# Kernel optimization log

Measured on AMD Instinct MI355X. Metric: run time of the kernel, lower is better.

## Reference

```python
import jax, jax.numpy as jnp
import numpy as np

TEMPERATURE = 0.5
BN_EPS = 1e-5
L2_EPS = 1e-12

B, D_IN, D_HID, D_OUT = 4096, 192, 512, 128


def setup_inputs() -> dict:
    key = jax.random.key(0)
    ks = jax.random.split(key, 4)
    return {
        "h1": jax.random.normal(ks[0], (B, D_IN), dtype=jnp.float32),
        "h2": jax.random.normal(ks[1], (B, D_IN), dtype=jnp.float32),
        "W1": jax.random.normal(ks[2], (D_HID, D_IN), dtype=jnp.float32) * (1.0 / np.sqrt(D_IN)),
        "b1": jnp.zeros((D_HID,), dtype=jnp.float32),
        "gamma": jnp.ones((D_HID,), dtype=jnp.float32),
        "beta": jnp.zeros((D_HID,), dtype=jnp.float32),
        "W2": jax.random.normal(ks[3], (D_OUT, D_HID), dtype=jnp.float32) * (1.0 / np.sqrt(D_HID)),
        "b2": jnp.zeros((D_OUT,), dtype=jnp.float32),
    }


def _projection_head(h, W1, b1, gamma, beta, W2, b2):
    # Linear -> BatchNorm1d (training-mode batch stats) -> ReLU -> Linear
    y = h @ W1.T + b1  # (B, D_HID)
    mean = jnp.mean(y, axis=0)
    var = jnp.mean((y - mean) ** 2, axis=0)  # biased var, as torch BN uses for normalization
    y = (y - mean) * jax.lax.rsqrt(var + BN_EPS) * gamma + beta
    y = jax.nn.relu(y)
    return y @ W2.T + b2  # (B, D_OUT)


def _l2_normalize(z):
    n = jnp.sqrt(jnp.sum(z * z, axis=1, keepdims=True))
    return z / jnp.maximum(n, L2_EPS)


def reference(h1, h2, W1, b1, gamma, beta, W2, b2):
    z1 = _l2_normalize(_projection_head(h1, W1, b1, gamma, beta, W2, b2))
    z2 = _l2_normalize(_projection_head(h2, W1, b1, gamma, beta, W2, b2))

    # NT-Xent, fully vectorized (equivalent to the per-row torch loop):
    z = jnp.concatenate([z1, z2], axis=0)            # (2B, D)
    sim = (z @ z.T) / TEMPERATURE                    # (2B, 2B)
    n2 = z.shape[0]
    sim = jnp.where(jnp.eye(n2, dtype=bool), -jnp.inf, sim)
    # positive pair similarity: sim[i, i+B] and sim[i+B, i] == z1_i . z2_i / T
    pos = jnp.sum(z1 * z2, axis=1) / TEMPERATURE     # (B,)
    pos = jnp.concatenate([pos, pos])                # (2B,)
    # excluding index i from the row equals including it since diag is -inf
    lse = jax.nn.logsumexp(sim, axis=1)              # (2B,)
    loss = jnp.mean(lse - pos)
    return loss, z1, z2
```

## Files before the change

### kernel.cpp

```cpp
#include <hip/hip_runtime.h>


#define NB   4096
#define DIN  192
#define DHID 512
#define DOUT 128
#define N2   8192
#define NSPLIT 32
#define SIM_ITERS 16

typedef short short8 __attribute__((ext_vector_type(8)));
typedef float floatx4 __attribute__((ext_vector_type(4)));

__device__ inline float fast_exp2(float x) {
#if __has_builtin(__builtin_amdgcn_exp2f)
    return __builtin_amdgcn_exp2f(x);
#else
    return exp2f(x);
#endif
}

__device__ inline unsigned short bf16_rne(float x) {
    unsigned int u = __float_as_uint(x);
    return (unsigned short)((u + 0x7fffu + ((u >> 16) & 1u)) >> 16);
}

__global__ __launch_bounds__(256) void prep(
    const float* __restrict__ W1, const float* __restrict__ W2,
    unsigned short* __restrict__ W1b, unsigned short* __restrict__ W2b,
    float* __restrict__ psumc, float* __restrict__ psqc, float* __restrict__ out)
{
    const int NW1 = DHID * DIN / 4;
    const int NW2 = DOUT * DHID / 4;
    if (blockIdx.x == 160) {
        int t = threadIdx.x;
        for (int i = t; i < 1024; i += 256) { psumc[i] = 0.f; psqc[i] = 0.f; }
        if (t == 0) out[0] = 0.f;
        return;
    }
    int id = blockIdx.x * 256 + threadIdx.x;
    const float* src; unsigned short* dst; int off;
    if (id < NW1)            { src = W1; dst = W1b; off = id; }
    else if (id < NW1 + NW2) { src = W2; dst = W2b; off = id - NW1; }
    else return;
    float4 x = ((const float4*)src)[off];
    unsigned int p0 = bf16_rne(x.x) | ((unsigned int)bf16_rne(x.y) << 16);
    unsigned int p1 = bf16_rne(x.z) | ((unsigned int)bf16_rne(x.w) << 16);
    ((uint2*)dst)[off] = make_uint2(p0, p1);
}

__global__ __launch_bounds__(256) void gemm1_mfma(
    const float* __restrict__ h1, const float* __restrict__ h2,
    const unsigned short* __restrict__ W1b, const float* __restrict__ b1,
    float* __restrict__ Y, float* __restrict__ psumc, float* __restrict__ psqc)
{
    const int t = threadIdx.x;
    const int wave = t >> 6, lane = t & 63;
    const int quad = lane >> 4, l15 = lane & 15;
    const int mb = blockIdx.x;
    const int m0 = mb * 128 + wave * 32;
    const int n0 = blockIdx.y * 64;
    const int v  = (mb >= 32);

    short8 a[2][6];
    #pragma unroll
    for (int mt = 0; mt < 2; ++mt) {
        int row = m0 + mt * 16 + l15;
        const float* hsrc = (row < NB) ? (h1 + (size_t)row * DIN)
                                       : (h2 + (size_t)(row - NB) * DIN);
        #pragma unroll
        for (int kc = 0; kc < 6; ++kc) {
            const float4* p = (const float4*)(hsrc + kc * 32 + quad * 8);
            float4 x0 = p[0], x1 = p[1];
            float xs[8] = {x0.x,x0.y,x0.z,x0.w,x1.x,x1.y,x1.z,x1.w};
            #pragma unroll
            for (int j = 0; j < 8; ++j) a[mt][kc][j] = (short)bf16_rne(xs[j]);
        }
    }

    #pragma unroll
    for (int nt = 0; nt < 4; ++nt) {
        const int col = n0 + nt * 16 + l15;
        const short8* bptr = (const short8*)(W1b + (size_t)col * DIN + quad * 8);
        short8 b[6];
        #pragma unroll
        for (int kc = 0; kc < 6; ++kc) b[kc] = bptr[kc * 4];
        floatx4 acc[2] = {{0.f,0.f,0.f,0.f},{0.f,0.f,0.f,0.f}};
        #pragma unroll
        for (int kc = 0; kc < 6; ++kc)
            #pragma unroll
            for (int mt = 0; mt < 2; ++mt)
                acc[mt] = __builtin_amdgcn_mfma_f32_16x16x32_bf16(a[mt][kc], b[kc], acc[mt], 0,0,0);
        const float bias = b1[col];
        float cs = 0.f, cq = 0.f;
        #pragma unroll
        for (int mt = 0; mt < 2; ++mt)
            #pragma unroll
            for (int reg = 0; reg < 4; ++reg) {
                float y = acc[mt][reg] + bias;
                int row = m0 + mt * 16 + quad * 4 + reg;
                Y[(size_t)row * DHID + col] = y;
                cs += y; cq += y * y;
            }
        cs += __shfl_xor(cs, 16); cs += __shfl_xor(cs, 32);
        cq += __shfl_xor(cq, 16); cq += __shfl_xor(cq, 32);
        if (quad == 0) {
            atomicAdd(psumc + v * DHID + col, cs);
            atomicAdd(psqc  + v * DHID + col, cq);
        }
    }
}

#define ZSCALE 1.6986436f

__global__ __launch_bounds__(256) void gemm2_mfma(
    const float* __restrict__ Y, const unsigned short* __restrict__ W2b,
    const float* __restrict__ psumc, const float* __restrict__ psqc,
    const float* __restrict__ gamma, const float* __restrict__ beta,
    const float* __restrict__ b2,
    unsigned short* __restrict__ Zb, float* __restrict__ outz)
{
    __shared__ float sc_sh[DHID], sh_sh[DHID];
    __shared__ float sq_lds[4][16];
    const int t = threadIdx.x;
    const int wave = t >> 6, lane = t & 63;
    const int quad = lane >> 4, l15 = lane & 15;
    const int mtbase = blockIdx.x * 16;
    const int v = (mtbase >= NB);

    for (int c = t; c < DHID; c += 256) {
        float mean = psumc[v * DHID + c] * (1.0f / NB);
        float var  = psqc [v * DHID + c] * (1.0f / NB) - mean * mean;
        float rstd = rsqrtf(var + 1e-5f);
        float scv = gamma[c] * rstd;
        sc_sh[c] = scv;
        sh_sh[c] = beta[c] - mean * scv;
    }
    __syncthreads();

    const float* yrow = Y + (size_t)(mtbase + l15) * DHID;
    floatx4 acc[2] = {{0.f,0.f,0.f,0.f},{0.f,0.f,0.f,0.f}};
    for (int kc = 0; kc < 16; ++kc) {
        const int k = kc * 32 + quad * 8;
        float4 y0 = *(const float4*)(yrow + k);
        float4 y1 = *(const float4*)(yrow + k + 4);
        float4 s0 = *(const float4*)&sc_sh[k], s1 = *(const float4*)&sc_sh[k + 4];
        float4 h0 = *(const float4*)&sh_sh[k], h1v = *(const float4*)&sh_sh[k + 4];
        float xs[8];
        xs[0] = fmaxf(y0.x * s0.x + h0.x, 0.f);
        xs[1] = fmaxf(y0.y * s0.y + h0.y, 0.f);
        xs[2] = fmaxf(y0.z * s0.z + h0.z, 0.f);
        xs[3] = fmaxf(y0.w * s0.w + h0.w, 0.f);
        xs[4] = fmaxf(y1.x * s1.x + h1v.x, 0.f);
        xs[5] = fmaxf(y1.y * s1.y + h1v.y, 0.f);
        xs[6] = fmaxf(y1.z * s1.z + h1v.z, 0.f);
        xs[7] = fmaxf(y1.w * s1.w + h1v.w, 0.f);
        short8 a;
        #pragma unroll
        for (int j = 0; j < 8; ++j) a[j] = (short)bf16_rne(xs[j]);
        #pragma unroll
        for (int nt = 0; nt < 2; ++nt) {
            const int col = wave * 32 + nt * 16 + l15;
            short8 b = *(const short8*)(W2b + (size_t)col * DHID + k);
            acc[nt] = __builtin_amdgcn_mfma_f32_16x16x32_bf16(a, b, acc[nt], 0,0,0);
        }
    }
    float bias[2];
    #pragma unroll
    for (int nt = 0; nt < 2; ++nt) bias[nt] = b2[wave * 32 + nt * 16 + l15];

    float zv[4][2];
    #pragma unroll
    for (int reg = 0; reg < 4; ++reg) {
        float sq = 0.f;
        #pragma unroll
        for (int nt = 0; nt < 2; ++nt) {
            zv[reg][nt] = acc[nt][reg] + bias[nt];
            sq += zv[reg][nt] * zv[reg][nt];
        }
        sq += __shfl_xor(sq, 1); sq += __shfl_xor(sq, 2);
        sq += __shfl_xor(sq, 4); sq += __shfl_xor(sq, 8);
        if (l15 == 0) sq_lds[wave][quad * 4 + reg] = sq;
    }
    __syncthreads();
    #pragma unroll
    for (int reg = 0; reg < 4; ++reg) {
        float tot = sq_lds[0][quad * 4 + reg] + sq_lds[1][quad * 4 + reg]
                  + sq_lds[2][quad * 4 + reg] + sq_lds[3][quad * 4 + reg];
        float inv = 1.0f / fmaxf(sqrtf(tot), 1e-12f);
        const int row = mtbase + quad * 4 + reg;
        const size_t ob = (size_t)row * DOUT;
        #pragma unroll
        for (int nt = 0; nt < 2; ++nt) {
            const int col = wave * 32 + nt * 16 + l15;
            float z = zv[reg][nt] * inv;
            outz[ob + col] = z;
            Zb[ob + col] = bf16_rne(z * ZSCALE);
        }
    }
}

__global__ __launch_bounds__(256, 2) void sim_mfma(
    const unsigned short* __restrict__ Zb, float* __restrict__ psum)
{
    __shared__ unsigned char bsh[65536];
    const int t = threadIdx.x;
    const int wave = t >> 6, lane = t & 63;
    const int quad = lane >> 4, l15 = lane & 15;
    const int mbase = blockIdx.x * 128 + wave * 32;
    const int cs = blockIdx.y;
    const int cbase = cs * (N2 / NSPLIT);

    {
        const uint4* src = (const uint4*)(Zb + (size_t)cbase * DOUT);
        #pragma unroll
        for (int k = 0; k < 16; ++k) {
            int idx = t + k * 256;
            uint4 vv = src[idx];
            int row  = idx >> 4;
            int slot = idx & 15;
            *(uint4*)(bsh + row * 256 + ((slot ^ (row & 15)) << 4)) = vv;
        }
    }

    short8 a[2][4];
    #pragma unroll
    for (int at = 0; at < 2; ++at) {
        const short8* zra = (const short8*)(Zb + (size_t)(mbase + at * 16 + l15) * DOUT + quad * 8);
        #pragma unroll
        for (int kc = 0; kc < 4; ++kc) a[at][kc] = zra[kc * 4];
    }

    float rs[2][4];
    #pragma unroll
    for (int at = 0; at < 2; ++at)
        #pragma unroll
        for (int r = 0; r < 4; ++r) rs[at][r] = 0.f;

    __syncthreads();

    #pragma unroll 1
    for (int nt = 0; nt < SIM_ITERS; ++nt) {
        const int crow = nt * 16 + l15;
        short8 b[4];
        #pragma unroll
        for (int kc = 0; kc < 4; ++kc) {
            int slot = kc * 4 + quad;
            int boff = crow * 256 + ((slot ^ (crow & 15)) << 4);
            b[kc] = *(const short8*)(bsh + boff);
        }

        floatx4 acc[2] = {{0.f,0.f,0.f,0.f},{0.f,0.f,0.f,0.f}};
        #pragma unroll
        for (int kc = 0; kc < 4; ++kc)
            #pragma unroll
            for (int at = 0; at < 2; ++at)
                acc[at] = __builtin_amdgcn_mfma_f32_16x16x32_bf16(a[at][kc], b[kc], acc[at], 0, 0, 0);

        #pragma unroll
        for (int at = 0; at < 2; ++at)
            #pragma unroll
            for (int r = 0; r < 4; ++r)
                rs[at][r] += fast_exp2(acc[at][r]);
    }

    #pragma unroll
    for (int at = 0; at < 2; ++at) {
        const int gi0 = mbase + at * 16 + quad * 4;
        #pragma unroll
        for (int r = 0; r < 4; ++r) {
            float s = rs[at][r];
            s += __shfl_xor(s, 1);
            s += __shfl_xor(s, 2);
            s += __shfl_xor(s, 4);
            s += __shfl_xor(s, 8);
            if (l15 == 0) psum[(size_t)cs * N2 + gi0 + r] = s;
        }
    }
}

__global__ __launch_bounds__(256) void row_finalize(
    const unsigned short* __restrict__ Zb, const float* __restrict__ psum,
    float* __restrict__ out)
{
    const int t = threadIdx.x, wave = t >> 6, lane = t & 63;
    const int half = lane >> 5, l5 = lane & 31;
    const unsigned int* Z32 = (const unsigned int*)Zb;
    const int gw = blockIdx.x * 4 + wave;
    float accrv = 0.f;

    #pragma unroll 1
    for (int pp = 0; pp < 4; ++pp) {
        const int k = gw * 4 + pp;
        float s = psum[(size_t)l5 * N2 + k + half * NB];
        s += __shfl_xor(s, 1); s += __shfl_xor(s, 2); s += __shfl_xor(s, 4);
        s += __shfl_xor(s, 8); s += __shfl_xor(s, 16);
        unsigned int aw = Z32[(size_t)k * 64 + lane];
        unsigned int bw = Z32[(size_t)(k + NB) * 64 + lane];
        float alo = __uint_as_float(aw << 16), ahi = __uint_as_float(aw & 0xffff0000u);
        float blo = __uint_as_float(bw << 16), bhi = __uint_as_float(bw & 0xffff0000u);
        float d12 = alo * blo + ahi * bhi;
        float d11 = alo * alo + ahi * ahi;
        float d22 = blo * blo + bhi * bhi;
        #pragma unroll
        for (int m = 1; m <= 32; m <<= 1) {
            d12 += __shfl_xor(d12, m);
            d11 += __shfl_xor(d11, m);
            d22 += __shfl_xor(d22, m);
        }
        if (l5 == 0) {
            float dself = half ? d22 : d11;
            accrv += logf(s - fast_exp2(dself)) - d12 * 0.69314718f;
        }
    }
    accrv += __shfl_xor(accrv, 32);
    __shared__ float wsr[4];
    if (lane == 0) wsr[wave] = accrv;
    __syncthreads();
    if (t == 0)
        atomicAdd(out, (wsr[0] + wsr[1] + wsr[2] + wsr[3]) * (1.0f / N2));
}

extern "C" void kernel_launch(void* const* d_in, const int* in_sizes, int n_in,
                              void* d_out, int out_size, void* d_ws, size_t ws_size,
                              hipStream_t stream)
{
    const float* h1    = (const float*)d_in[0];
    const float* h2    = (const float*)d_in[1];
    const float* W1    = (const float*)d_in[2];
    const float* b1    = (const float*)d_in[3];
    const float* gamma = (const float*)d_in[4];
    const float* beta  = (const float*)d_in[5];
    const float* W2    = (const float*)d_in[6];
    const float* b2    = (const float*)d_in[7];
    float* out = (float*)d_out;

    float* ws      = (float*)d_ws;
    float* psumc   = ws;
    float* psqc    = psumc + 1024;
    unsigned short* W1b = (unsigned short*)(psqc + 1024);
    unsigned short* W2b = W1b + DHID * DIN;
    float* Y       = (float*)(W2b + DOUT * DHID);
    float* psum    = Y + (size_t)N2 * DHID;
    unsigned short* Zb = (unsigned short*)(psum + (size_t)NSPLIT * N2);

    prep        <<<dim3(161),        256, 0, stream>>>(W1, W2, W1b, W2b, psumc, psqc, out);
    gemm1_mfma  <<<dim3(64, 8),      256, 0, stream>>>(h1, h2, W1b, b1, Y, psumc, psqc);
    gemm2_mfma  <<<dim3(512),        256, 0, stream>>>(Y, W2b, psumc, psqc, gamma, beta, b2, Zb, out + 1);
    sim_mfma    <<<dim3(64, NSPLIT), 256, 0, stream>>>(Zb, psum);
    row_finalize<<<dim3(256),        256, 0, stream>>>(Zb, psum, out);
}
```

Baseline: 141.4 us.

## Exploit symmetry of similarity matrix to compute only upper-triangular tiles

The similarity kernel now iterates over upper-triangular 256x256 super-tile pairs instead of the full 8192x8192 grid. Each off-diagonal tile adds its exp values both to its row sums and, through an LDS column reduction, to the column sums of the mirrored rows. Results are accumulated with atomics into a single per-row sum buffer, which removes the split partial-sum array and its reduction in the finalize kernel. This roughly halves the MFMA and exp work, at the cost of extra shuffles, LDS updates, atomics and float summation order that is no longer deterministic.

```diff
diff --git a/kernel.cpp b/kernel.cpp
--- a/kernel.cpp
+++ b/kernel.cpp
@@ -6,7 +6,7 @@
 #define DHID 512
 #define DOUT 128
 #define N2   8192
-#define NSPLIT 32
+#define NSUPER 32
 #define SIM_ITERS 16
 
 typedef short short8 __attribute__((ext_vector_type(8)));
@@ -28,13 +28,15 @@
 __global__ __launch_bounds__(256) void prep(
     const float* __restrict__ W1, const float* __restrict__ W2,
     unsigned short* __restrict__ W1b, unsigned short* __restrict__ W2b,
-    float* __restrict__ psumc, float* __restrict__ psqc, float* __restrict__ out)
+    float* __restrict__ psumc, float* __restrict__ psqc,
+    float* __restrict__ out, float* __restrict__ psum_row)
 {
     const int NW1 = DHID * DIN / 4;
     const int NW2 = DOUT * DHID / 4;
     if (blockIdx.x == 160) {
         int t = threadIdx.x;
         for (int i = t; i < 1024; i += 256) { psumc[i] = 0.f; psqc[i] = 0.f; }
+        for (int i = t; i < N2; i += 256)   psum_row[i] = 0.f;
         if (t == 0) out[0] = 0.f;
         return;
     }
@@ -201,15 +203,29 @@
 }
 
 __global__ __launch_bounds__(256, 2) void sim_mfma(
-    const unsigned short* __restrict__ Zb, float* __restrict__ psum)
+    const unsigned short* __restrict__ Zb, float* __restrict__ psum_row)
 {
     __shared__ unsigned char bsh[65536];
+    __shared__ float colsum[4][256];
     const int t = threadIdx.x;
     const int wave = t >> 6, lane = t & 63;
     const int quad = lane >> 4, l15 = lane & 15;
-    const int mbase = blockIdx.x * 128 + wave * 32;
-    const int cs = blockIdx.y;
-    const int cbase = cs * (N2 / NSPLIT);
+
+    int R, C, half;
+    {
+        int id = blockIdx.x;
+        if (id < 2 * NSUPER) { R = id >> 1; C = R; half = id & 1; }
+        else {
+            int p2 = id - 2 * NSUPER;
+            int pair = p2 >> 1; half = p2 & 1;
+            int r = 0, rem = pair;
+            while (rem >= NSUPER - 1 - r) { rem -= NSUPER - 1 - r; ++r; }
+            R = r; C = r + 1 + rem;
+        }
+    }
+    const bool docol = (C != R);
+    const int mbase = R * 256 + half * 128 + wave * 32;
+    const int cbase = C * 256;
 
     {
         const uint4* src = (const uint4*)(Zb + (size_t)cbase * DOUT);
@@ -221,6 +237,8 @@
             int slot = idx & 15;
             *(uint4*)(bsh + row * 256 + ((slot ^ (row & 15)) << 4)) = vv;
         }
+        #pragma unroll
+        for (int w = 0; w < 4; ++w) colsum[w][t] = 0.f;
     }
 
     short8 a[2][4];
@@ -257,12 +275,23 @@
             for (int at = 0; at < 2; ++at)
                 acc[at] = __builtin_amdgcn_mfma_f32_16x16x32_bf16(a[at][kc], b[kc], acc[at], 0, 0, 0);
 
+        float cst = 0.f;
         #pragma unroll
         for (int at = 0; at < 2; ++at)
             #pragma unroll
-            for (int r = 0; r < 4; ++r)
-                rs[at][r] += fast_exp2(acc[at][r]);
-    }
+            for (int r = 0; r < 4; ++r) {
+                float e = fast_exp2(acc[at][r]);
+                rs[at][r] += e;
+                cst += e;
+            }
+        if (docol) {
+            cst += __shfl_xor(cst, 16);
+            cst += __shfl_xor(cst, 32);
+            if (quad == 0) colsum[wave][nt * 16 + l15] += cst;
+        }
+    }
+
+    __syncthreads();
 
     #pragma unroll
     for (int at = 0; at < 2; ++at) {
@@ -274,13 +303,17 @@
             s += __shfl_xor(s, 2);
             s += __shfl_xor(s, 4);
             s += __shfl_xor(s, 8);
-            if (l15 == 0) psum[(size_t)cs * N2 + gi0 + r] = s;
-        }
+            if (l15 == 0) atomicAdd(psum_row + gi0 + r, s);
+        }
+    }
+    if (docol) {
+        float tot = colsum[0][t] + colsum[1][t] + colsum[2][t] + colsum[3][t];
+        atomicAdd(psum_row + cbase + t, tot);
     }
 }
 
 __global__ __launch_bounds__(256) void row_finalize(
-    const unsigned short* __restrict__ Zb, const float* __restrict__ psum,
+    const unsigned short* __restrict__ Zb, const float* __restrict__ psum_row,
     float* __restrict__ out)
 {
     const int t = threadIdx.x, wave = t >> 6, lane = t & 63;
@@ -292,9 +325,6 @@
     #pragma unroll 1
     for (int pp = 0; pp < 4; ++pp) {
         const int k = gw * 4 + pp;
-        float s = psum[(size_t)l5 * N2 + k + half * NB];
-        s += __shfl_xor(s, 1); s += __shfl_xor(s, 2); s += __shfl_xor(s, 4);
-        s += __shfl_xor(s, 8); s += __shfl_xor(s, 16);
         unsigned int aw = Z32[(size_t)k * 64 + lane];
         unsigned int bw = Z32[(size_t)(k + NB) * 64 + lane];
         float alo = __uint_as_float(aw << 16), ahi = __uint_as_float(aw & 0xffff0000u);
@@ -309,6 +339,7 @@
             d22 += __shfl_xor(d22, m);
         }
         if (l5 == 0) {
+            float s = psum_row[k + half * NB];
             float dself = half ? d22 : d11;
             accrv += logf(s - fast_exp2(dself)) - d12 * 0.69314718f;
         }
@@ -341,12 +372,14 @@
     unsigned short* W1b = (unsigned short*)(psqc + 1024);
     unsigned short* W2b = W1b + DHID * DIN;
     float* Y       = (float*)(W2b + DOUT * DHID);
-    float* psum    = Y + (size_t)N2 * DHID;
-    unsigned short* Zb = (unsigned short*)(psum + (size_t)NSPLIT * N2);
-
-    prep        <<<dim3(161),        256, 0, stream>>>(W1, W2, W1b, W2b, psumc, psqc, out);
+    float* psum_row= Y + (size_t)N2 * DHID;
+    unsigned short* Zb = (unsigned short*)(psum_row + N2);
+
+    const int SIM_BLOCKS = 2 * NSUPER + (NSUPER * (NSUPER - 1) / 2) * 2;
+
+    prep        <<<dim3(161),        256, 0, stream>>>(W1, W2, W1b, W2b, psumc, psqc, out, psum_row);
     gemm1_mfma  <<<dim3(64, 8),      256, 0, stream>>>(h1, h2, W1b, b1, Y, psumc, psqc);
     gemm2_mfma  <<<dim3(512),        256, 0, stream>>>(Y, W2b, psumc, psqc, gamma, beta, b2, Zb, out + 1);
-    sim_mfma    <<<dim3(64, NSPLIT), 256, 0, stream>>>(Zb, psum);
-    row_finalize<<<dim3(256),        256, 0, stream>>>(Zb, psum, out);
-}
+    sim_mfma    <<<dim3(SIM_BLOCKS), 256, 0, stream>>>(Zb, psum_row);
+    row_finalize<<<dim3(256),        256, 0, stream>>>(Zb, psum_row, out);
+}
```

New measurement: 141.2 us. No clear change (-0.2%).

## Double-buffer column tile in LDS to cut shared memory and overlap loads

Applied to the files above, without the earlier changes.

The sim kernel now stages its 256-row column slice in four 64-row chunks through a 2x16KB double buffer instead of one 64KB load. The next chunk's global loads are issued into registers before the MFMA/exp work on the current chunk, and the launch bound rises to 4 blocks per CU. The goal is to hide global load latency and raise occupancy. In exchange it adds two barriers per chunk and more register pressure from the prefetch registers.

```diff
diff --git a/kernel.cpp b/kernel.cpp
--- a/kernel.cpp
+++ b/kernel.cpp
@@ -200,10 +200,10 @@
     }
 }
 
-__global__ __launch_bounds__(256, 2) void sim_mfma(
+__global__ __launch_bounds__(256, 4) void sim_mfma(
     const unsigned short* __restrict__ Zb, float* __restrict__ psum)
 {
-    __shared__ unsigned char bsh[65536];
+    __shared__ unsigned char bsh[2][16384];
     const int t = threadIdx.x;
     const int wave = t >> 6, lane = t & 63;
     const int quad = lane >> 4, l15 = lane & 15;
@@ -211,24 +211,24 @@
     const int cs = blockIdx.y;
     const int cbase = cs * (N2 / NSPLIT);
 
+    short8 a[2][4];
+    #pragma unroll
+    for (int at = 0; at < 2; ++at) {
+        const short8* zra = (const short8*)(Zb + (size_t)(mbase + at * 16 + l15) * DOUT + quad * 8);
+        #pragma unroll
+        for (int kc = 0; kc < 4; ++kc) a[at][kc] = zra[kc * 4];
+    }
+
     {
         const uint4* src = (const uint4*)(Zb + (size_t)cbase * DOUT);
         #pragma unroll
-        for (int k = 0; k < 16; ++k) {
+        for (int k = 0; k < 4; ++k) {
             int idx = t + k * 256;
             uint4 vv = src[idx];
-            int row  = idx >> 4;
+            int lr  = idx >> 4;
             int slot = idx & 15;
-            *(uint4*)(bsh + row * 256 + ((slot ^ (row & 15)) << 4)) = vv;
-        }
-    }
-
-    short8 a[2][4];
-    #pragma unroll
-    for (int at = 0; at < 2; ++at) {
-        const short8* zra = (const short8*)(Zb + (size_t)(mbase + at * 16 + l15) * DOUT + quad * 8);
-        #pragma unroll
-        for (int kc = 0; kc < 4; ++kc) a[at][kc] = zra[kc * 4];
+            *(uint4*)(&bsh[0][lr * 256 + ((slot ^ (lr & 15)) << 4)]) = vv;
+        }
     }
 
     float rs[2][4];
@@ -239,29 +239,48 @@
 
     __syncthreads();
 
-    #pragma unroll 1
-    for (int nt = 0; nt < SIM_ITERS; ++nt) {
-        const int crow = nt * 16 + l15;
-        short8 b[4];
-        #pragma unroll
-        for (int kc = 0; kc < 4; ++kc) {
-            int slot = kc * 4 + quad;
-            int boff = crow * 256 + ((slot ^ (crow & 15)) << 4);
-            b[kc] = *(const short8*)(bsh + boff);
-        }
-
-        floatx4 acc[2] = {{0.f,0.f,0.f,0.f},{0.f,0.f,0.f,0.f}};
-        #pragma unroll
-        for (int kc = 0; kc < 4; ++kc)
+    #pragma unroll
+    for (int c = 0; c < 4; ++c) {
+        uint4 pre[4];
+        if (c < 3) {
+            const uint4* src = (const uint4*)(Zb + (size_t)(cbase + (c + 1) * 64) * DOUT);
+            #pragma unroll
+            for (int k = 0; k < 4; ++k) pre[k] = src[t + k * 256];
+        }
+
+        #pragma unroll
+        for (int i = 0; i < 4; ++i) {
+            const int lr = i * 16 + l15;
+            short8 b[4];
+            #pragma unroll
+            for (int kc = 0; kc < 4; ++kc) {
+                int slot = kc * 4 + quad;
+                b[kc] = *(const short8*)(&bsh[c & 1][lr * 256 + ((slot ^ (lr & 15)) << 4)]);
+            }
+            floatx4 acc[2] = {{0.f,0.f,0.f,0.f},{0.f,0.f,0.f,0.f}};
+            #pragma unroll
+            for (int kc = 0; kc < 4; ++kc)
+                #pragma unroll
+                for (int at = 0; at < 2; ++at)
+                    acc[at] = __builtin_amdgcn_mfma_f32_16x16x32_bf16(a[at][kc], b[kc], acc[at], 0, 0, 0);
             #pragma unroll
             for (int at = 0; at < 2; ++at)
-                acc[at] = __builtin_amdgcn_mfma_f32_16x16x32_bf16(a[at][kc], b[kc], acc[at], 0, 0, 0);
-
-        #pragma unroll
-        for (int at = 0; at < 2; ++at)
-            #pragma unroll
-            for (int r = 0; r < 4; ++r)
-                rs[at][r] += fast_exp2(acc[at][r]);
+                #pragma unroll
+                for (int r = 0; r < 4; ++r)
+                    rs[at][r] += fast_exp2(acc[at][r]);
+        }
+
+        if (c < 3) {
+            __syncthreads();
+            #pragma unroll
+            for (int k = 0; k < 4; ++k) {
+                int idx = t + k * 256;
+                int lr  = idx >> 4;
+                int slot = idx & 15;
+                *(uint4*)(&bsh[(c + 1) & 1][lr * 256 + ((slot ^ (lr & 15)) << 4)]) = pre[k];
+            }
+            __syncthreads();
+        }
     }
 
     #pragma unroll
```

Measured after the change: 177.6 us. 25.6% more time.
